# Kernel optimization log

Measured on AMD Instinct MI355X. Metric: run time of the kernel, lower is better.

## Reference

```python
import jax, jax.numpy as jnp
import numpy as np

BN_EPS = 1e-5

def _square_distance(src, dst):
    # src: (B,N,3), dst: (B,S,3) -> (B,N,S)
    d = -2.0 * jnp.einsum('bnc,bsc->bns', src, dst)
    d = d + jnp.sum(src * src, -1)[:, :, None]
    d = d + jnp.sum(dst * dst, -1)[:, None, :]
    return d

def _bn_relu(x, gamma, beta):
    # x: (B,N,C); training-mode batchnorm over (B,N)
    mean = jnp.mean(x, axis=(0, 1))
    var = jnp.mean(jnp.square(x - mean), axis=(0, 1))
    y = (x - mean) * jax.lax.rsqrt(var + BN_EPS) * gamma + beta
    return jax.nn.relu(y)

def setup_inputs() -> dict:
    key = jax.random.key(0)
    ks = jax.random.split(key, 12)
    B, N, S, D1, D2 = 8, 8192, 2048, 128, 256
    in_ch, mlp = 384, [256, 256]
    inp = {
        'xyz1': jax.random.normal(ks[0], (B, 3, N), jnp.float32),
        'xyz2': jax.random.normal(ks[1], (B, 3, S), jnp.float32),
        'points1': jax.random.normal(ks[2], (B, D1, N), jnp.float32),
        'points2': jax.random.normal(ks[3], (B, D2, S), jnp.float32),
    }
    last = in_ch
    for i, out in enumerate(mlp):
        inp[f'W{i+1}'] = jax.random.normal(ks[4 + 2 * i], (out, last), jnp.float32) * (1.0 / np.sqrt(last))
        inp[f'b{i+1}'] = jnp.zeros((out,), jnp.float32)
        inp[f'g{i+1}'] = jnp.ones((out,), jnp.float32)
        inp[f'beta{i+1}'] = jnp.zeros((out,), jnp.float32)
        last = out
    return inp

def reference(xyz1, xyz2, points1, points2, W1, b1, g1, beta1, W2, b2, g2, beta2):
    p1 = jnp.transpose(xyz1, (0, 2, 1))   # (B,N,3)
    p2 = jnp.transpose(xyz2, (0, 2, 1))   # (B,S,3)
    f2 = jnp.transpose(points2, (0, 2, 1))  # (B,S,D2)

    dists = _square_distance(p1, p2)      # (B,N,S)
    neg_d, idx = jax.lax.top_k(-dists, 3)  # 3 smallest distances
    d3 = -neg_d                            # (B,N,3)
    dist_recip = 1.0 / (d3 + 1e-8)
    weight = dist_recip / jnp.sum(dist_recip, axis=2, keepdims=True)  # (B,N,3)

    gathered = jax.vmap(lambda p, i: p[i])(f2, idx)   # (B,N,3,D2)
    interp = jnp.sum(gathered * weight[..., None], axis=2)  # (B,N,D2)

    f1 = jnp.transpose(points1, (0, 2, 1))  # (B,N,D1)
    x = jnp.concatenate([f1, interp], axis=-1)  # (B,N,D1+D2)

    x = _bn_relu(jnp.einsum('bnc,oc->bno', x, W1) + b1, g1, beta1)
    x = _bn_relu(jnp.einsum('bnc,oc->bno', x, W2) + b2, g2, beta2)
    return jnp.transpose(x, (0, 2, 1))  # (B,256,N)
```

## Files before the change

### kernel.cpp

```cpp
#include <hip/hip_runtime.h>

#define B_   8
#define N_   8192
#define S_   2048
#define D1_  128
#define D2_  256
#define O_   256
#define BN_  (B_*N_)

typedef __bf16 bf16;
typedef __bf16 bf16x8_t __attribute__((ext_vector_type(8)));
typedef __bf16 bf16x4_t __attribute__((ext_vector_type(4)));
typedef float  f32x4_t  __attribute__((ext_vector_type(4)));

static const size_t OFF_IDX  = 0;
static const size_t OFF_W    = 786432;
static const size_t OFF_XP   = 1572864;
static const size_t OFF_Z    = 51904512;
static const size_t OFF_SS1  = 85458944;
static const size_t OFF_SS2  = 85460992;
static const size_t OFF_PART = 85463040;

#define GL16(gsrc, ldst) \
  __builtin_amdgcn_global_load_lds((const __attribute__((address_space(1))) void*)(gsrc), \
                                   (__attribute__((address_space(3))) void*)(ldst), 16, 0, 0)

__global__ __launch_bounds__(256) void k_conv_p1(const float* __restrict__ p1, bf16* __restrict__ xp) {
  const int g  = blockIdx.x * 256 + threadIdx.x;
  const int n4 = g & 2047;
  const int c8 = (g >> 11) & 15;
  const int b  = g >> 15;
  const int n  = n4 * 4;
  const float* src = p1 + ((size_t)b * D1_ + c8 * 8) * N_ + n;
  bf16x8_t o0, o1, o2, o3;
  #pragma unroll
  for (int j = 0; j < 8; ++j) {
    float4 v = *(const float4*)(src + (size_t)j * N_);
    o0[j] = (bf16)v.x; o1[j] = (bf16)v.y; o2[j] = (bf16)v.z; o3[j] = (bf16)v.w;
  }
  bf16* dst = xp + (((size_t)b * 48 + c8) * N_ + n) * 8;
  *(bf16x8_t*)(dst)      = o0;
  *(bf16x8_t*)(dst + 8)  = o1;
  *(bf16x8_t*)(dst + 16) = o2;
  *(bf16x8_t*)(dst + 24) = o3;
}

__device__ __forceinline__ void ins3(float d, int i,
                                     float& d0, float& d1, float& d2,
                                     int& i0, int& i1, int& i2) {
  const bool c2 = d < d2, c1 = d < d1, c0 = d < d0;
  const float nd2 = c1 ? d1 : (c2 ? d : d2); const int ni2 = c1 ? i1 : (c2 ? i : i2);
  const float nd1 = c0 ? d0 : (c1 ? d : d1); const int ni1 = c0 ? i0 : (c1 ? i : i1);
  d0 = c0 ? d : d0; i0 = c0 ? i : i0;
  d1 = nd1; i1 = ni1; d2 = nd2; i2 = ni2;
}

__global__ __launch_bounds__(256) void k_nn3(const float* __restrict__ xyz1, const float* __restrict__ xyz2,
                                             int* __restrict__ idxw, float* __restrict__ www) {
  __shared__ float4 sq[4][S_ / 4];
  __shared__ float  pd[4][64][3];
  __shared__ int    pi[4][64][3];
  const int tid  = threadIdx.x;
  const int lane = tid & 63, w = tid >> 6;
  const int b     = blockIdx.y;
  const int nbase = blockIdx.x * 64;

  const float* x2 = xyz2 + (size_t)b * 3 * S_;
  for (int j = tid; j < S_ / 4; j += 256) {
    const float4 x = *(const float4*)(x2 + 4 * j);
    const float4 y = *(const float4*)(x2 + S_ + 4 * j);
    const float4 z = *(const float4*)(x2 + 2 * S_ + 4 * j);
    float4 qq;
    qq.x = fmaf(x.x, x.x, fmaf(y.x, y.x, z.x * z.x));
    qq.y = fmaf(x.y, x.y, fmaf(y.y, y.y, z.y * z.y));
    qq.z = fmaf(x.z, x.z, fmaf(y.z, y.z, z.z * z.z));
    qq.w = fmaf(x.w, x.w, fmaf(y.w, y.w, z.w * z.w));
    sq[0][j] = x; sq[1][j] = y; sq[2][j] = z; sq[3][j] = qq;
  }

  const int n = nbase + lane;
  const float* x1 = xyz1 + (size_t)b * 3 * N_;
  const float px = x1[n], py = x1[N_ + n], pz = x1[2 * N_ + n];
  const float ax = -2.f * px, ay = -2.f * py, az = -2.f * pz;
  __syncthreads();

  float e0 = 3.4e38f, e1 = 3.4e38f, e2 = 3.4e38f;
  int   i0 = 0, i1 = 0, i2 = 0;

  const int jb = w * (S_ / 16);
  #pragma unroll 4
  for (int j = jb; j < jb + S_ / 16; ++j) {
    const float4 qx = sq[0][j], qy = sq[1][j], qz = sq[2][j], qq = sq[3][j];
    #define CAND(C, SI)                                                        \
      {                                                                        \
        const float E = fmaf(ax, qx.C, fmaf(ay, qy.C, fmaf(az, qz.C, qq.C))); \
        const bool l0 = E < e0, l1 = E < e1, l2 = E < e2;                      \
        const int ni1 = l0 ? i0 : (l1 ? (SI) : i1);                            \
        const int ni2 = l1 ? i1 : (l2 ? (SI) : i2);                            \
        i0 = l0 ? (SI) : i0; i1 = ni1; i2 = ni2;                               \
        const float ne1 = __builtin_amdgcn_fmed3f(E, e0, e1);                  \
        const float ne2 = __builtin_amdgcn_fmed3f(E, e1, e2);                  \
        e0 = fminf(E, e0); e1 = ne1; e2 = ne2;                                 \
      }
    CAND(x, 4 * j + 0)
    CAND(y, 4 * j + 1)
    CAND(z, 4 * j + 2)
    CAND(w, 4 * j + 3)
    #undef CAND
  }

  const float pp = fmaf(px, px, fmaf(py, py, pz * pz));
  pd[w][lane][0] = e0 + pp; pd[w][lane][1] = e1 + pp; pd[w][lane][2] = e2 + pp;
  pi[w][lane][0] = i0; pi[w][lane][1] = i1; pi[w][lane][2] = i2;
  __syncthreads();

  if (tid < 64) {
    float d0 = pd[0][tid][0], d1 = pd[0][tid][1], d2 = pd[0][tid][2];
    int   j0 = pi[0][tid][0], j1 = pi[0][tid][1], j2 = pi[0][tid][2];
    #pragma unroll
    for (int ck = 1; ck < 4; ++ck)
      #pragma unroll
      for (int k = 0; k < 3; ++k)
        ins3(pd[ck][tid][k], pi[ck][tid][k], d0, d1, d2, j0, j1, j2);
    const float r0 = 1.f / (d0 + 1e-8f), r1 = 1.f / (d1 + 1e-8f), r2 = 1.f / (d2 + 1e-8f);
    const float inv = 1.f / (r0 + r1 + r2);
    const int bn = b * N_ + nbase + tid;
    idxw[bn] = j0; idxw[BN_ + bn] = j1; idxw[2 * BN_ + bn] = j2;
    www[bn] = r0 * inv; www[BN_ + bn] = r1 * inv; www[2 * BN_ + bn] = r2 * inv;
  }
}

__global__ __launch_bounds__(256) void k_t2(const float* __restrict__ p2, bf16* __restrict__ f2t) {
  __shared__ float lds[64][65];
  const int bid = blockIdx.x;
  const int b = bid & 7;
  const int inner = bid >> 3;
  const int s0 = (inner & 31) * 64;
  const int c0 = (inner >> 5) * 64;
  const int t = threadIdx.x;
  {
    const int cr = t >> 2, scb = (t & 3) * 16;
    const float* src = p2 + ((size_t)b * D2_ + c0 + cr) * S_ + s0 + scb;
    #pragma unroll
    for (int i = 0; i < 4; ++i) {
      const float4 v = *(const float4*)(src + 4 * i);
      lds[cr][scb + 4 * i + 0] = v.x; lds[cr][scb + 4 * i + 1] = v.y;
      lds[cr][scb + 4 * i + 2] = v.z; lds[cr][scb + 4 * i + 3] = v.w;
    }
  }
  __syncthreads();
  const int co = (t & 7) * 8;
  #pragma unroll
  for (int pass = 0; pass < 2; ++pass) {
    const int s = pass * 32 + (t >> 3);
    bf16x8_t o;
    #pragma unroll
    for (int j = 0; j < 8; ++j) o[j] = (bf16)lds[co + j][s];
    *(bf16x8_t*)(f2t + ((size_t)b * S_ + s0 + s) * D2_ + c0 + co) = o;
  }
}

__global__ __launch_bounds__(256) void k_interp(const bf16* __restrict__ f2t, const int* __restrict__ idxw,
                                                const float* __restrict__ www, bf16* __restrict__ xp) {
  const int bid = blockIdx.x;
  const int b = bid & 7;
  const int n = (bid >> 3) * 8 + (threadIdx.x & 7);
  const int c8 = threadIdx.x >> 3;
  const int bn = b * N_ + n;
  const int j0 = idxw[bn], j1 = idxw[BN_ + bn], j2 = idxw[2 * BN_ + bn];
  const float w0 = www[bn], w1 = www[BN_ + bn], w2 = www[2 * BN_ + bn];
  const bf16* base = f2t + (size_t)b * S_ * D2_ + c8 * 8;
  const bf16x8_t v0 = *(const bf16x8_t*)(base + (size_t)j0 * D2_);
  const bf16x8_t v1 = *(const bf16x8_t*)(base + (size_t)j1 * D2_);
  const bf16x8_t v2 = *(const bf16x8_t*)(base + (size_t)j2 * D2_);
  bf16x8_t out;
  #pragma unroll
  for (int j = 0; j < 8; ++j)
    out[j] = (bf16)(w0 * (float)v0[j] + w1 * (float)v1[j] + w2 * (float)v2[j]);
  *(bf16x8_t*)(xp + (((size_t)b * 48 + 16 + c8) * N_ + (size_t)n) * 8) = out;
}

__global__ __launch_bounds__(256) void k_wprep(const float* __restrict__ W1, const float* __restrict__ W2,
                                               bf16* __restrict__ img) {
  const int g = blockIdx.x * 256 + threadIdx.x;
  if (g < 12288) {
    const int e = g * 8;
    const int imgblk = e >> 12, r = e & 4095;
    const int kc = r >> 10, row = (r & 1023) >> 3;
    const int mblk = imgblk / 12, kt32 = imgblk % 12;
    const float* s = W1 + (size_t)(mblk * 128 + row) * 384 + kt32 * 32 + kc * 8;
    const float4 f0 = *(const float4*)(s), f1 = *(const float4*)(s + 4);
    bf16x8_t h;
    h[0] = (bf16)f0.x; h[1] = (bf16)f0.y; h[2] = (bf16)f0.z; h[3] = (bf16)f0.w;
    h[4] = (bf16)f1.x; h[5] = (bf16)f1.y; h[6] = (bf16)f1.z; h[7] = (bf16)f1.w;
    *(bf16x8_t*)(img + e) = h;
  } else if (g < 20480) {
    const int e = (g - 12288) * 8;
    const int imgblk = e >> 12, r = e & 4095;
    const int kc = r >> 10, row = (r & 1023) >> 3;
    const int mblk = imgblk >> 3, kt32 = imgblk & 7;
    const float* s = W2 + (size_t)(mblk * 128 + row) * 256 + kt32 * 32 + kc * 8;
    const float4 f0 = *(const float4*)(s), f1 = *(const float4*)(s + 4);
    bf16x8_t h;
    h[0] = (bf16)f0.x; h[1] = (bf16)f0.y; h[2] = (bf16)f0.z; h[3] = (bf16)f0.w;
    h[4] = (bf16)f1.x; h[5] = (bf16)f1.y; h[6] = (bf16)f1.z; h[7] = (bf16)f1.w;
    *(bf16x8_t*)(img + 98304 + e) = h;
  }
}

template<int K>
__global__ __launch_bounds__(256) void k_gemm(const bf16* __restrict__ Wimg, const float* __restrict__ bias,
                                              const bf16* __restrict__ X, bf16* __restrict__ Zp) {
  __shared__ bf16 As[4096];
  __shared__ bf16 Bt[4096];
  const int tid = threadIdx.x;
  const int lane = tid & 63, wid = tid >> 6;
  const int wr = wid >> 1, wc = wid & 1;
  const int dd = blockIdx.x;
  const int xcd = dd & 7, pos = dd >> 3;
  const int b = pos >> 4, q = pos & 15;
  const int m0 = (q & 1) * 128;
  const int n0 = (xcd * 8 + (q >> 1)) * 128;
  const int mblk = m0 >> 7;
  const int l15 = lane & 15, l4 = lane >> 4;

  f32x4_t acc[4][4];
  #pragma unroll
  for (int i = 0; i < 4; ++i)
    #pragma unroll
    for (int j = 0; j < 4; ++j) { f32x4_t z = {0.f, 0.f, 0.f, 0.f}; acc[i][j] = z; }

  const bf16* Xb = X + (size_t)b * (K / 8) * ((size_t)N_ * 8);

  for (int kt = 0; kt < K; kt += 32) {
    const bf16* asrc = Wimg + (size_t)(mblk * (K / 32) + (kt >> 5)) * 4096 + wid * 1024 + lane * 8;
    GL16(asrc,       &As[wid * 1024]);
    GL16(asrc + 512, &As[wid * 1024 + 512]);
    const bf16* bsrc = Xb + ((size_t)(kt >> 3) + wid) * ((size_t)N_ * 8) + ((size_t)n0 + lane) * 8;
    GL16(bsrc,       &Bt[wid * 1024]);
    GL16(bsrc + 512, &Bt[wid * 1024 + 512]);
    __syncthreads();
    bf16x8_t af[4], bfr[4];
    #pragma unroll
    for (int mi = 0; mi < 4; ++mi) af[mi]  = *(const bf16x8_t*)&As[l4 * 1024 + (wr * 64 + mi * 16 + l15) * 8];
    #pragma unroll
    for (int ni = 0; ni < 4; ++ni) bfr[ni] = *(const bf16x8_t*)&Bt[l4 * 1024 + (wc * 64 + ni * 16 + l15) * 8];
    #pragma unroll
    for (int mi = 0; mi < 4; ++mi)
      #pragma unroll
      for (int ni = 0; ni < 4; ++ni)
        acc[mi][ni] = __builtin_amdgcn_mfma_f32_16x16x32_bf16(af[mi], bfr[ni], acc[mi][ni], 0, 0, 0);
    __syncthreads();
  }
  bf16* Zb = Zp + (size_t)b * 32 * ((size_t)N_ * 8);
  #pragma unroll
  for (int mi = 0; mi < 4; ++mi) {
    const int obase = m0 + wr * 64 + mi * 16 + l4 * 4;
    const float4 bv = *(const float4*)(bias + obase);
    const size_t gofs = (size_t)(obase >> 3) * ((size_t)N_ * 8) + (obase & 7);
    #pragma unroll
    for (int ni = 0; ni < 4; ++ni) {
      const int nn = n0 + wc * 64 + ni * 16 + l15;
      bf16x4_t o;
      o[0] = (bf16)(acc[mi][ni][0] + bv.x);
      o[1] = (bf16)(acc[mi][ni][1] + bv.y);
      o[2] = (bf16)(acc[mi][ni][2] + bv.z);
      o[3] = (bf16)(acc[mi][ni][3] + bv.w);
      *(bf16x4_t*)(Zb + gofs + (size_t)nn * 8) = o;
    }
  }
}

__global__ __launch_bounds__(256) void k_stats_p(const bf16* __restrict__ Z, float* __restrict__ part) {
  const int og = blockIdx.x & 31, b = blockIdx.x >> 5;
  const bf16* src = Z + ((size_t)b * 32 + og) * ((size_t)N_ * 8);
  float s[8], q[8];
  #pragma unroll
  for (int j = 0; j < 8; ++j) { s[j] = 0.f; q[j] = 0.f; }
  for (int n = threadIdx.x; n < N_; n += 256) {
    const bf16x8_t v = *(const bf16x8_t*)(src + (size_t)n * 8);
    #pragma unroll
    for (int j = 0; j < 8; ++j) {
      const float f = (float)v[j];
      s[j] += f; q[j] = fmaf(f, f, q[j]);
    }
  }
  #pragma unroll
  for (int off = 1; off < 64; off <<= 1) {
    #pragma unroll
    for (int j = 0; j < 8; ++j) {
      s[j] += __shfl_xor(s[j], off);
      q[j] += __shfl_xor(q[j], off);
    }
  }
  __shared__ float red[4][16];
  const int w = threadIdx.x >> 6;
  if ((threadIdx.x & 63) == 0) {
    #pragma unroll
    for (int j = 0; j < 8; ++j) { red[w][j] = s[j]; red[w][8 + j] = q[j]; }
  }
  __syncthreads();
  if (threadIdx.x < 16) {
    const float t = red[0][threadIdx.x] + red[1][threadIdx.x] + red[2][threadIdx.x] + red[3][threadIdx.x];
    const int sel = threadIdx.x >> 3, j = threadIdx.x & 7;
    part[((size_t)sel * 256 + og * 8 + j) * 8 + b] = t;
  }
}

__global__ __launch_bounds__(256) void k_ss(const float* __restrict__ part, const float* __restrict__ g,
                                            const float* __restrict__ be, float* __restrict__ ss) {
  const int c = threadIdx.x;
  float s = 0.f, q = 0.f;
  #pragma unroll
  for (int b = 0; b < 8; ++b) { s += part[(size_t)c * 8 + b]; q += part[(256 + (size_t)c) * 8 + b]; }
  const float mean = s * (1.f / 65536.f);
  const float var  = q * (1.f / 65536.f) - mean * mean;
  const float rstd = rsqrtf(var + 1e-5f);
  const float sc = g[c] * rstd;
  ss[c] = sc; ss[O_ + c] = be[c] - mean * sc;
}

__global__ __launch_bounds__(256) void k_apply_p(bf16* __restrict__ Z, const float* __restrict__ ss) {
  const int nc = blockIdx.x & 31, og = (blockIdx.x >> 5) & 31, b = blockIdx.x >> 10;
  const int n = nc * 256 + threadIdx.x;
  bf16* p = Z + (((size_t)b * 32 + og) * N_ + n) * 8;
  bf16x8_t v = *(bf16x8_t*)p;
  #pragma unroll
  for (int j = 0; j < 8; ++j) {
    const int c = og * 8 + j;
    v[j] = (bf16)fmaxf(fmaf((float)v[j], ss[c], ss[O_ + c]), 0.f);
  }
  *(bf16x8_t*)p = v;
}

__global__ __launch_bounds__(256) void k_final_p(const bf16* __restrict__ Z, const float* __restrict__ ss,
                                                 float* __restrict__ Y) {
  const int b  = blockIdx.x >> 7;
  const int n0 = (blockIdx.x & 127) * 64;
  const int og = threadIdx.x >> 3, ns = threadIdx.x & 7;
  const bf16* src = Z + (((size_t)b * 32 + og) * N_ + n0 + ns * 8) * 8;
  bf16x8_t v[8];
  #pragma unroll
  for (int i = 0; i < 8; ++i) v[i] = *(const bf16x8_t*)(src + i * 8);
  float sc[8], sh[8];
  #pragma unroll
  for (int j = 0; j < 8; ++j) { sc[j] = ss[og * 8 + j]; sh[j] = ss[O_ + og * 8 + j]; }
  float* dst = Y + ((size_t)b * O_ + og * 8) * N_ + n0 + ns * 8;
  #pragma unroll
  for (int j = 0; j < 8; ++j) {
    float4 a0, a1;
    a0.x = fmaxf(fmaf((float)v[0][j], sc[j], sh[j]), 0.f);
    a0.y = fmaxf(fmaf((float)v[1][j], sc[j], sh[j]), 0.f);
    a0.z = fmaxf(fmaf((float)v[2][j], sc[j], sh[j]), 0.f);
    a0.w = fmaxf(fmaf((float)v[3][j], sc[j], sh[j]), 0.f);
    a1.x = fmaxf(fmaf((float)v[4][j], sc[j], sh[j]), 0.f);
    a1.y = fmaxf(fmaf((float)v[5][j], sc[j], sh[j]), 0.f);
    a1.z = fmaxf(fmaf((float)v[6][j], sc[j], sh[j]), 0.f);
    a1.w = fmaxf(fmaf((float)v[7][j], sc[j], sh[j]), 0.f);
    *(float4*)(dst + (size_t)j * N_)     = a0;
    *(float4*)(dst + (size_t)j * N_ + 4) = a1;
  }
}

extern "C" void kernel_launch(void* const* d_in, const int* in_sizes, int n_in,
                              void* d_out, int out_size, void* d_ws, size_t ws_size,
                              hipStream_t stream) {
  const float* xyz1    = (const float*)d_in[0];
  const float* xyz2    = (const float*)d_in[1];
  const float* points1 = (const float*)d_in[2];
  const float* points2 = (const float*)d_in[3];
  const float* W1  = (const float*)d_in[4];
  const float* b1  = (const float*)d_in[5];
  const float* g1  = (const float*)d_in[6];
  const float* be1 = (const float*)d_in[7];
  const float* W2  = (const float*)d_in[8];
  const float* b2  = (const float*)d_in[9];
  const float* g2  = (const float*)d_in[10];
  const float* be2 = (const float*)d_in[11];
  float* Y = (float*)d_out;
  char*  ws = (char*)d_ws;
  int*   idxw  = (int*)(ws + OFF_IDX);
  float* www   = (float*)(ws + OFF_W);
  bf16*  wimg1 = (bf16*)(ws + OFF_IDX);
  bf16*  wimg2 = wimg1 + 98304;
  bf16*  xp    = (bf16*)(ws + OFF_XP);
  bf16*  z1    = (bf16*)(ws + OFF_Z);
  bf16*  f2t   = (bf16*)(ws + OFF_Z);
  bf16*  z2    = (bf16*)(ws + OFF_XP);
  float* ss1   = (float*)(ws + OFF_SS1);
  float* ss2   = (float*)(ws + OFF_SS2);
  float* part  = (float*)(ws + OFF_PART);

  hipLaunchKernelGGL(k_conv_p1, dim3(1024), dim3(256), 0, stream, points1, xp);
  hipLaunchKernelGGL(k_nn3, dim3(128, 8), dim3(256), 0, stream, xyz1, xyz2, idxw, www);
  hipLaunchKernelGGL(k_t2, dim3(1024), dim3(256), 0, stream, points2, f2t);
  hipLaunchKernelGGL(k_interp, dim3(8192), dim3(256), 0, stream, f2t, idxw, www, xp);
  hipLaunchKernelGGL(k_wprep, dim3(80), dim3(256), 0, stream, W1, W2, wimg1);
  hipLaunchKernelGGL((k_gemm<384>), dim3(1024), dim3(256), 0, stream, wimg1, b1, xp, z1);
  hipLaunchKernelGGL(k_stats_p, dim3(256), dim3(256), 0, stream, z1, part);
  hipLaunchKernelGGL(k_ss, dim3(1), dim3(256), 0, stream, part, g1, be1, ss1);
  hipLaunchKernelGGL(k_apply_p, dim3(8192), dim3(256), 0, stream, z1, ss1);
  hipLaunchKernelGGL((k_gemm<256>), dim3(1024), dim3(256), 0, stream, wimg2, b2, z1, z2);
  hipLaunchKernelGGL(k_stats_p, dim3(256), dim3(256), 0, stream, z2, part);
  hipLaunchKernelGGL(k_ss, dim3(1), dim3(256), 0, stream, part, g2, be2, ss2);
  hipLaunchKernelGGL(k_final_p, dim3(1024), dim3(256), 0, stream, z2, ss2, Y);
}
```

Before: 190.8 us.

## Replace brute-force 3-NN with z-binned spatial search and pruning

Adds a per-batch kernel that buckets xyz2 points into 64 z-slabs (counting sort), then rewrites the 3-NN kernel to search outward from the query's slab and stop once the slab distance exceeds the current third-best distance. The goal is to avoid evaluating all 2048 candidates per query point. It packs distance and index into 64-bit keys for the top-3 selection. In exchange it adds an extra launch and divergent, data-dependent loops, and the pruning gain depends on the point distribution. Ties are broken by index, and distances are now computed directly rather than through the expanded-norm formula, so they may differ slightly from the reference.

```diff
diff --git a/kernel.cpp b/kernel.cpp
--- a/kernel.cpp
+++ b/kernel.cpp
@@ -45,87 +45,139 @@
   *(bf16x8_t*)(dst + 24) = o3;
 }
 
-__device__ __forceinline__ void ins3(float d, int i,
-                                     float& d0, float& d1, float& d2,
-                                     int& i0, int& i1, int& i2) {
-  const bool c2 = d < d2, c1 = d < d1, c0 = d < d0;
-  const float nd2 = c1 ? d1 : (c2 ? d : d2); const int ni2 = c1 ? i1 : (c2 ? i : i2);
-  const float nd1 = c0 ? d0 : (c1 ? d : d1); const int ni1 = c0 ? i0 : (c1 ? i : i1);
-  d0 = c0 ? d : d0; i0 = c0 ? i : i0;
-  d1 = nd1; i1 = ni1; d2 = nd2; i2 = ni2;
-}
-
-__global__ __launch_bounds__(256) void k_nn3(const float* __restrict__ xyz1, const float* __restrict__ xyz2,
+__global__ __launch_bounds__(256) void k_sortz(const float* __restrict__ xyz2,
+                                               float4* __restrict__ srt, int* __restrict__ hdr) {
+  __shared__ float zl[S_];
+  __shared__ int cnt[64], cnt2[64], starts[65];
+  __shared__ float rmin[4], rmax[4];
+  const int b = blockIdx.x, tid = threadIdx.x;
+  const float* z2 = xyz2 + (size_t)b * 3 * S_ + 2 * S_;
+  float lmin = 3.4e38f, lmax = -3.4e38f;
+  for (int i = tid; i < S_; i += 256) {
+    const float z = z2[i]; zl[i] = z;
+    lmin = fminf(lmin, z); lmax = fmaxf(lmax, z);
+  }
+  #pragma unroll
+  for (int off = 32; off; off >>= 1) {
+    lmin = fminf(lmin, __shfl_down(lmin, off));
+    lmax = fmaxf(lmax, __shfl_down(lmax, off));
+  }
+  if ((tid & 63) == 0) { rmin[tid >> 6] = lmin; rmax[tid >> 6] = lmax; }
+  if (tid < 64) { cnt[tid] = 0; cnt2[tid] = 0; }
+  __syncthreads();
+  const float zmin = fminf(fminf(rmin[0], rmin[1]), fminf(rmin[2], rmin[3]));
+  const float zmax = fmaxf(fmaxf(rmax[0], rmax[1]), fmaxf(rmax[2], rmax[3]));
+  const float scale = 63.999f / fmaxf(zmax - zmin, 1e-20f);
+  for (int i = tid; i < S_; i += 256) {
+    const int bi = min(63, max(0, (int)((zl[i] - zmin) * scale)));
+    atomicAdd(&cnt[bi], 1);
+  }
+  __syncthreads();
+  if (tid == 0) {
+    int acc = 0;
+    for (int k = 0; k < 64; ++k) { starts[k] = acc; acc += cnt[k]; }
+    starts[64] = acc;
+  }
+  __syncthreads();
+  const float* x2 = xyz2 + (size_t)b * 3 * S_;
+  const float* y2 = x2 + S_;
+  for (int i = tid; i < S_; i += 256) {
+    const float z = zl[i];
+    const int bi = min(63, max(0, (int)((z - zmin) * scale)));
+    const int pos = starts[bi] + atomicAdd(&cnt2[bi], 1);
+    float4 o; o.x = x2[i]; o.y = y2[i]; o.z = z; o.w = __uint_as_float((unsigned)i);
+    srt[(size_t)b * S_ + pos] = o;
+  }
+  if (tid < 65) hdr[b * 68 + tid] = starts[tid];
+  if (tid == 0) { hdr[b * 68 + 65] = __float_as_int(zmin); hdr[b * 68 + 66] = __float_as_int(scale); }
+}
+
+__global__ __launch_bounds__(256) void k_nn3(const float* __restrict__ xyz1, const float4* __restrict__ srt_g,
+                                             const int* __restrict__ hdr,
                                              int* __restrict__ idxw, float* __restrict__ www) {
-  __shared__ float4 sq[4][S_ / 4];
-  __shared__ float  pd[4][64][3];
-  __shared__ int    pi[4][64][3];
-  const int tid  = threadIdx.x;
-  const int lane = tid & 63, w = tid >> 6;
-  const int b     = blockIdx.y;
-  const int nbase = blockIdx.x * 64;
-
-  const float* x2 = xyz2 + (size_t)b * 3 * S_;
-  for (int j = tid; j < S_ / 4; j += 256) {
-    const float4 x = *(const float4*)(x2 + 4 * j);
-    const float4 y = *(const float4*)(x2 + S_ + 4 * j);
-    const float4 z = *(const float4*)(x2 + 2 * S_ + 4 * j);
-    float4 qq;
-    qq.x = fmaf(x.x, x.x, fmaf(y.x, y.x, z.x * z.x));
-    qq.y = fmaf(x.y, x.y, fmaf(y.y, y.y, z.y * z.y));
-    qq.z = fmaf(x.z, x.z, fmaf(y.z, y.z, z.z * z.z));
-    qq.w = fmaf(x.w, x.w, fmaf(y.w, y.w, z.w * z.w));
-    sq[0][j] = x; sq[1][j] = y; sq[2][j] = z; sq[3][j] = qq;
-  }
+  __shared__ float4 srt[S_];
+  __shared__ int starts_l[65];
+  __shared__ unsigned long long pk[4][64][3];
+  const int tid = threadIdx.x, lane = tid & 63, w = tid >> 6;
+  const int b = blockIdx.y, nbase = blockIdx.x * 64;
+
+  const float4* sg = srt_g + (size_t)b * S_;
+  for (int i = tid; i < S_; i += 256) srt[i] = sg[i];
+  if (tid < 65) starts_l[tid] = hdr[b * 68 + tid];
+  const float zmin  = __int_as_float(hdr[b * 68 + 65]);
+  const float scale = __int_as_float(hdr[b * 68 + 66]);
 
   const int n = nbase + lane;
   const float* x1 = xyz1 + (size_t)b * 3 * N_;
   const float px = x1[n], py = x1[N_ + n], pz = x1[2 * N_ + n];
-  const float ax = -2.f * px, ay = -2.f * py, az = -2.f * pz;
-  __syncthreads();
-
-  float e0 = 3.4e38f, e1 = 3.4e38f, e2 = 3.4e38f;
-  int   i0 = 0, i1 = 0, i2 = 0;
-
-  const int jb = w * (S_ / 16);
-  #pragma unroll 4
-  for (int j = jb; j < jb + S_ / 16; ++j) {
-    const float4 qx = sq[0][j], qy = sq[1][j], qz = sq[2][j], qq = sq[3][j];
-    #define CAND(C, SI)                                                        \
-      {                                                                        \
-        const float E = fmaf(ax, qx.C, fmaf(ay, qy.C, fmaf(az, qz.C, qq.C))); \
-        const bool l0 = E < e0, l1 = E < e1, l2 = E < e2;                      \
-        const int ni1 = l0 ? i0 : (l1 ? (SI) : i1);                            \
-        const int ni2 = l1 ? i1 : (l2 ? (SI) : i2);                            \
-        i0 = l0 ? (SI) : i0; i1 = ni1; i2 = ni2;                               \
-        const float ne1 = __builtin_amdgcn_fmed3f(E, e0, e1);                  \
-        const float ne2 = __builtin_amdgcn_fmed3f(E, e1, e2);                  \
-        e0 = fminf(E, e0); e1 = ne1; e2 = ne2;                                 \
-      }
-    CAND(x, 4 * j + 0)
-    CAND(y, 4 * j + 1)
-    CAND(z, 4 * j + 2)
-    CAND(w, 4 * j + 3)
-    #undef CAND
-  }
-
-  const float pp = fmaf(px, px, fmaf(py, py, pz * pz));
-  pd[w][lane][0] = e0 + pp; pd[w][lane][1] = e1 + pp; pd[w][lane][2] = e2 + pp;
-  pi[w][lane][0] = i0; pi[w][lane][1] = i1; pi[w][lane][2] = i2;
+  __syncthreads();
+
+  const float winv   = 1.f / scale;
+  const float winv_p = winv * 1.000002f;
+  const float winv_m = winv * 0.999998f;
+  const int qb = min(63, max(0, (int)((pz - zmin) * scale)));
+
+  unsigned long long k0 = 0x7F7FFFFFFFFFFFFFull, k1 = k0, k2 = k0;
+
+  int lo = qb, hi = qb, cur = qb;
+  bool have = true;
+  for (int round = 0; round < 66; ++round) {
+    const int curc = min(63, max(0, cur));
+    const int s = starts_l[curc];
+    const int cnt = have ? (starts_l[curc + 1] - s) : 0;
+    for (int t = 0; ; ++t) {
+      const int e = w + 4 * t;
+      const bool v = e < cnt;
+      if (!__any(v)) break;
+      const float4 c = srt[s + (v ? e : 0)];
+      const float dx = px - c.x, dy = py - c.y, dzv = pz - c.z;
+      const float d = fmaf(dx, dx, fmaf(dy, dy, dzv * dzv));
+      unsigned long long key = ((unsigned long long)__float_as_uint(d) << 32)
+                             | (unsigned long long)__float_as_uint(c.w);
+      if (!v) key = ~0ull;
+      const bool c0 = key < k0, c1 = key < k1, c2 = key < k2;
+      const unsigned long long n1 = c0 ? k0 : (c1 ? key : k1);
+      const unsigned long long n2 = c1 ? k1 : (c2 ? key : k2);
+      k0 = c0 ? key : k0; k1 = n1; k2 = n2;
+    }
+    const float d2  = __uint_as_float((unsigned)(k2 >> 32));
+    const float dzl = (lo > 0)  ? (pz - fmaf((float)lo, winv_p, zmin)) : 3.4e38f;
+    const float dzr = (hi < 63) ? (fmaf((float)(hi + 1), winv_m, zmin) - pz) : 3.4e38f;
+    const bool goL = (lo > 0)  && (dzl * dzl <= d2);
+    const bool goR = (hi < 63) && (dzr * dzr <= d2);
+    const bool pickL = goL && (!goR || dzl <= dzr);
+    const bool pickR = goR && !pickL;
+    have = pickL || pickR;
+    cur = pickL ? (lo - 1) : (hi + 1);
+    lo -= pickL ? 1 : 0;
+    hi += pickR ? 1 : 0;
+    if (!__any(have)) break;
+  }
+
+  pk[w][lane][0] = k0; pk[w][lane][1] = k1; pk[w][lane][2] = k2;
   __syncthreads();
 
   if (tid < 64) {
-    float d0 = pd[0][tid][0], d1 = pd[0][tid][1], d2 = pd[0][tid][2];
-    int   j0 = pi[0][tid][0], j1 = pi[0][tid][1], j2 = pi[0][tid][2];
+    unsigned long long m0 = pk[0][tid][0], m1 = pk[0][tid][1], m2 = pk[0][tid][2];
     #pragma unroll
     for (int ck = 1; ck < 4; ++ck)
       #pragma unroll
-      for (int k = 0; k < 3; ++k)
-        ins3(pd[ck][tid][k], pi[ck][tid][k], d0, d1, d2, j0, j1, j2);
+      for (int k = 0; k < 3; ++k) {
+        const unsigned long long key = pk[ck][tid][k];
+        const bool c0 = key < m0, c1 = key < m1, c2 = key < m2;
+        const unsigned long long n1 = c0 ? m0 : (c1 ? key : m1);
+        const unsigned long long n2 = c1 ? m1 : (c2 ? key : m2);
+        m0 = c0 ? key : m0; m1 = n1; m2 = n2;
+      }
+    const float d0 = __uint_as_float((unsigned)(m0 >> 32));
+    const float d1 = __uint_as_float((unsigned)(m1 >> 32));
+    const float d2 = __uint_as_float((unsigned)(m2 >> 32));
     const float r0 = 1.f / (d0 + 1e-8f), r1 = 1.f / (d1 + 1e-8f), r2 = 1.f / (d2 + 1e-8f);
     const float inv = 1.f / (r0 + r1 + r2);
     const int bn = b * N_ + nbase + tid;
-    idxw[bn] = j0; idxw[BN_ + bn] = j1; idxw[2 * BN_ + bn] = j2;
+    idxw[bn]           = (int)(unsigned)(m0 & 0xFFFFFFFFull);
+    idxw[BN_ + bn]     = (int)(unsigned)(m1 & 0xFFFFFFFFull);
+    idxw[2 * BN_ + bn] = (int)(unsigned)(m2 & 0xFFFFFFFFull);
     www[bn] = r0 * inv; www[BN_ + bn] = r1 * inv; www[2 * BN_ + bn] = r2 * inv;
   }
 }
@@ -384,6 +436,8 @@
   bf16*  wimg1 = (bf16*)(ws + OFF_IDX);
   bf16*  wimg2 = wimg1 + 98304;
   bf16*  xp    = (bf16*)(ws + OFF_XP);
+  float4* srt  = (float4*)(ws + OFF_Z);
+  int*    hdr  = (int*)(ws + OFF_Z + 262144);
   bf16*  z1    = (bf16*)(ws + OFF_Z);
   bf16*  f2t   = (bf16*)(ws + OFF_Z);
   bf16*  z2    = (bf16*)(ws + OFF_XP);
@@ -392,7 +446,8 @@
   float* part  = (float*)(ws + OFF_PART);
 
   hipLaunchKernelGGL(k_conv_p1, dim3(1024), dim3(256), 0, stream, points1, xp);
-  hipLaunchKernelGGL(k_nn3, dim3(128, 8), dim3(256), 0, stream, xyz1, xyz2, idxw, www);
+  hipLaunchKernelGGL(k_sortz, dim3(8), dim3(256), 0, stream, xyz2, srt, hdr);
+  hipLaunchKernelGGL(k_nn3, dim3(128, 8), dim3(256), 0, stream, xyz1, srt, hdr, idxw, www);
   hipLaunchKernelGGL(k_t2, dim3(1024), dim3(256), 0, stream, points2, f2t);
   hipLaunchKernelGGL(k_interp, dim3(8192), dim3(256), 0, stream, f2t, idxw, www, xp);
   hipLaunchKernelGGL(k_wprep, dim3(80), dim3(256), 0, stream, W1, W2, wimg1);
```

After: 286.5 us. +50.2%, slower.

## Replace brute-force 3-NN with z-slab binned search over sorted points

Applied to the files above, without the earlier changes.

Adds two kernels that counting-sort reference and query points into 64 z-slabs per batch, then rewrites the 3-NN kernel so each wavefront scans only a window of slabs near its sorted queries. The window expands until the third-best distance proves no closer point can exist outside it. This removes most of the all-pairs distance work, at the cost of two extra small-grid sort kernels with serial per-thread loops and some wavefront divergence in the window expansion.

```diff
diff --git a/kernel.cpp b/kernel.cpp
--- a/kernel.cpp
+++ b/kernel.cpp
@@ -17,6 +17,9 @@
 static const size_t OFF_W    = 786432;
 static const size_t OFF_XP   = 1572864;
 static const size_t OFF_Z    = 51904512;
+static const size_t OFF_CS   = OFF_Z;
+static const size_t OFF_HDR  = OFF_Z + 327680;
+static const size_t OFF_QS   = OFF_Z + 331776;
 static const size_t OFF_SS1  = 85458944;
 static const size_t OFF_SS2  = 85460992;
 static const size_t OFF_PART = 85463040;
@@ -45,89 +48,209 @@
   *(bf16x8_t*)(dst + 24) = o3;
 }
 
-__device__ __forceinline__ void ins3(float d, int i,
-                                     float& d0, float& d1, float& d2,
-                                     int& i0, int& i1, int& i2) {
-  const bool c2 = d < d2, c1 = d < d1, c0 = d < d0;
-  const float nd2 = c1 ? d1 : (c2 ? d : d2); const int ni2 = c1 ? i1 : (c2 ? i : i2);
-  const float nd1 = c0 ? d0 : (c1 ? d : d1); const int ni1 = c0 ? i0 : (c1 ? i : i1);
-  d0 = c0 ? d : d0; i0 = c0 ? i : i0;
-  d1 = nd1; i1 = ni1; d2 = nd2; i2 = ni2;
-}
-
-__global__ __launch_bounds__(256) void k_nn3(const float* __restrict__ xyz1, const float* __restrict__ xyz2,
+__global__ __launch_bounds__(256) void k_sortz(const float* __restrict__ xyz2,
+                                               float* __restrict__ cs, int* __restrict__ hdr) {
+  __shared__ float zl[S_];
+  __shared__ unsigned short h[64][257];
+  __shared__ int starts[65];
+  __shared__ float mm[8];
+  const int b = blockIdx.x, t = threadIdx.x;
+  const float* x2 = xyz2 + (size_t)b * 3 * S_;
+  const float* y2 = x2 + S_;
+  const float* z2 = x2 + 2 * S_;
+  float lmin = 3.4e38f, lmax = -3.4e38f;
+  for (int i = t; i < S_; i += 256) {
+    const float z = z2[i]; zl[i] = z;
+    lmin = fminf(lmin, z); lmax = fmaxf(lmax, z);
+  }
+  #pragma unroll
+  for (int off = 32; off; off >>= 1) {
+    lmin = fminf(lmin, __shfl_down(lmin, off));
+    lmax = fmaxf(lmax, __shfl_down(lmax, off));
+  }
+  if ((t & 63) == 0) { mm[t >> 6] = lmin; mm[4 + (t >> 6)] = lmax; }
+  unsigned short* hf = &h[0][0];
+  for (int i = t; i < 64 * 257; i += 256) hf[i] = 0;
+  __syncthreads();
+  const float zmin  = fminf(fminf(mm[0], mm[1]), fminf(mm[2], mm[3]));
+  const float zmax  = fmaxf(fmaxf(mm[4], mm[5]), fmaxf(mm[6], mm[7]));
+  const float scale = 63.999f / fmaxf(zmax - zmin, 1e-20f);
+  #pragma unroll
+  for (int k = 0; k < 8; ++k) {
+    const int i = t * 8 + k;
+    const int bi = min(63, (int)((zl[i] - zmin) * scale));
+    h[bi][t]++;
+  }
+  __syncthreads();
+  if (t < 64) {
+    int run = 0;
+    for (int tt = 0; tt < 256; ++tt) { const int c = h[t][tt]; h[t][tt] = (unsigned short)run; run += c; }
+    starts[t] = run;
+  }
+  __syncthreads();
+  if (t == 0) {
+    int acc = 0;
+    for (int k = 0; k < 64; ++k) { const int c = starts[k]; starts[k] = acc; acc += c; }
+    starts[64] = acc;
+  }
+  __syncthreads();
+  float* xs = cs + (size_t)b * 5 * S_;
+  float* ys = xs + S_; float* zs = ys + S_; float* qs = zs + S_; float* ids = qs + S_;
+  #pragma unroll
+  for (int k = 0; k < 8; ++k) {
+    const int i = t * 8 + k;
+    const float z = zl[i];
+    const int bi = min(63, (int)((z - zmin) * scale));
+    const int pos = starts[bi] + h[bi][t]; h[bi][t]++;
+    const float x = x2[i], y = y2[i];
+    xs[pos] = x; ys[pos] = y; zs[pos] = z;
+    qs[pos] = fmaf(x, x, fmaf(y, y, z * z));
+    ids[pos] = __uint_as_float((unsigned)i);
+  }
+  if (t < 65) hdr[b * 68 + t] = starts[t];
+  if (t == 0) { hdr[b * 68 + 65] = __float_as_int(zmin); hdr[b * 68 + 66] = __float_as_int(scale); }
+}
+
+__global__ __launch_bounds__(256) void k_sortq(const float* __restrict__ xyz1, float4* __restrict__ qsrt) {
+  __shared__ unsigned short h[64][257];
+  __shared__ int starts[65];
+  __shared__ float mm[8];
+  const int b = blockIdx.x, t = threadIdx.x;
+  const float* x1 = xyz1 + (size_t)b * 3 * N_;
+  const float* y1 = x1 + N_;
+  const float* z1 = x1 + 2 * N_;
+  float lmin = 3.4e38f, lmax = -3.4e38f;
+  for (int i = t; i < N_; i += 256) {
+    const float z = z1[i];
+    lmin = fminf(lmin, z); lmax = fmaxf(lmax, z);
+  }
+  #pragma unroll
+  for (int off = 32; off; off >>= 1) {
+    lmin = fminf(lmin, __shfl_down(lmin, off));
+    lmax = fmaxf(lmax, __shfl_down(lmax, off));
+  }
+  if ((t & 63) == 0) { mm[t >> 6] = lmin; mm[4 + (t >> 6)] = lmax; }
+  unsigned short* hf = &h[0][0];
+  for (int i = t; i < 64 * 257; i += 256) hf[i] = 0;
+  __syncthreads();
+  const float zmin  = fminf(fminf(mm[0], mm[1]), fminf(mm[2], mm[3]));
+  const float zmax  = fmaxf(fmaxf(mm[4], mm[5]), fmaxf(mm[6], mm[7]));
+  const float scale = 63.999f / fmaxf(zmax - zmin, 1e-20f);
+  for (int k = 0; k < 32; ++k) {
+    const int i = t * 32 + k;
+    const int bi = min(63, (int)((z1[i] - zmin) * scale));
+    h[bi][t]++;
+  }
+  __syncthreads();
+  if (t < 64) {
+    int run = 0;
+    for (int tt = 0; tt < 256; ++tt) { const int c = h[t][tt]; h[t][tt] = (unsigned short)run; run += c; }
+    starts[t] = run;
+  }
+  __syncthreads();
+  if (t == 0) {
+    int acc = 0;
+    for (int k = 0; k < 64; ++k) { const int c = starts[k]; starts[k] = acc; acc += c; }
+    starts[64] = acc;
+  }
+  __syncthreads();
+  for (int k = 0; k < 32; ++k) {
+    const int i = t * 32 + k;
+    const float z = z1[i];
+    const int bi = min(63, (int)((z - zmin) * scale));
+    const int pos = starts[bi] + h[bi][t]; h[bi][t]++;
+    float4 o; o.x = x1[i]; o.y = y1[i]; o.z = z; o.w = __uint_as_float((unsigned)i);
+    qsrt[(size_t)b * N_ + pos] = o;
+  }
+}
+
+#define CAND(C, SI)                                                            \
+  {                                                                            \
+    const float E = fmaf(ax, qx.C, fmaf(ay, qy.C, fmaf(az, qz.C, qv.C)));      \
+    const bool l0 = E < e0, l1 = E < e1, l2 = E < e2;                          \
+    const int t1 = l0 ? s0 : (l1 ? (SI) : s1);                                 \
+    const int t2 = l1 ? s1 : (l2 ? (SI) : s2);                                 \
+    s0 = l0 ? (SI) : s0; s1 = t1; s2 = t2;                                     \
+    const float m1 = __builtin_amdgcn_fmed3f(E, e0, e1);                       \
+    const float m2 = __builtin_amdgcn_fmed3f(E, e1, e2);                       \
+    e0 = fminf(E, e0); e1 = m1; e2 = m2;                                       \
+  }
+#define SCAN_RANGE(GA, GB)                                                     \
+  for (int j_ = (GA); j_ < (GB); ++j_) {                                       \
+    const float4 qx = sq[0][j_], qy = sq[1][j_], qz = sq[2][j_], qv = sq[3][j_]; \
+    CAND(x, 4 * j_)                                                            \
+    CAND(y, 4 * j_ + 1)                                                        \
+    CAND(z, 4 * j_ + 2)                                                        \
+    CAND(w, 4 * j_ + 3)                                                        \
+  }
+
+__global__ __launch_bounds__(256) void k_nn3(const float4* __restrict__ qsrt, const float* __restrict__ cs,
+                                             const int* __restrict__ hdr,
                                              int* __restrict__ idxw, float* __restrict__ www) {
-  __shared__ float4 sq[4][S_ / 4];
-  __shared__ float  pd[4][64][3];
-  __shared__ int    pi[4][64][3];
-  const int tid  = threadIdx.x;
-  const int lane = tid & 63, w = tid >> 6;
-  const int b     = blockIdx.y;
-  const int nbase = blockIdx.x * 64;
-
-  const float* x2 = xyz2 + (size_t)b * 3 * S_;
-  for (int j = tid; j < S_ / 4; j += 256) {
-    const float4 x = *(const float4*)(x2 + 4 * j);
-    const float4 y = *(const float4*)(x2 + S_ + 4 * j);
-    const float4 z = *(const float4*)(x2 + 2 * S_ + 4 * j);
-    float4 qq;
-    qq.x = fmaf(x.x, x.x, fmaf(y.x, y.x, z.x * z.x));
-    qq.y = fmaf(x.y, x.y, fmaf(y.y, y.y, z.y * z.y));
-    qq.z = fmaf(x.z, x.z, fmaf(y.z, y.z, z.z * z.z));
-    qq.w = fmaf(x.w, x.w, fmaf(y.w, y.w, z.w * z.w));
-    sq[0][j] = x; sq[1][j] = y; sq[2][j] = z; sq[3][j] = qq;
-  }
-
-  const int n = nbase + lane;
-  const float* x1 = xyz1 + (size_t)b * 3 * N_;
-  const float px = x1[n], py = x1[N_ + n], pz = x1[2 * N_ + n];
+  __shared__ float4 sq[5][512];
+  __shared__ int starts_l[65];
+  const int tid = threadIdx.x;
+  const int b = blockIdx.y, qbase = blockIdx.x * 256;
+
+  const float4* cs4 = (const float4*)(cs + (size_t)b * 5 * S_);
+  for (int g = tid; g < 5 * 512; g += 256) sq[g >> 9][g & 511] = cs4[g];
+  if (tid < 65) starts_l[tid] = hdr[b * 68 + tid];
+  const float zmin  = __int_as_float(hdr[b * 68 + 65]);
+  const float scale = __int_as_float(hdr[b * 68 + 66]);
+
+  const float4 q = qsrt[(size_t)b * N_ + qbase + tid];
+  const float px = q.x, py = q.y, pz = q.z;
+  const unsigned qn = __float_as_uint(q.w);
   const float ax = -2.f * px, ay = -2.f * py, az = -2.f * pz;
-  __syncthreads();
+  const float pp = fmaf(px, px, fmaf(py, py, pz * pz));
+  __syncthreads();
+
+  const float winv = 1.f / scale;
+  const int qb = min(63, max(0, (int)((pz - zmin) * scale)));
+  int loB = qb, hiB = qb;
+  while (loB > 0  && (starts_l[qb] - starts_l[loB])     < 256) --loB;
+  while (hiB < 63 && (starts_l[hiB + 1] - starts_l[qb + 1]) < 256) ++hiB;
+  #pragma unroll
+  for (int off = 1; off < 64; off <<= 1) {
+    loB = min(loB, __shfl_xor(loB, off));
+    hiB = max(hiB, __shfl_xor(hiB, off));
+  }
+  int gl = starts_l[loB] >> 2;
+  int gh = (starts_l[hiB + 1] + 3) >> 2;
 
   float e0 = 3.4e38f, e1 = 3.4e38f, e2 = 3.4e38f;
-  int   i0 = 0, i1 = 0, i2 = 0;
-
-  const int jb = w * (S_ / 16);
-  #pragma unroll 4
-  for (int j = jb; j < jb + S_ / 16; ++j) {
-    const float4 qx = sq[0][j], qy = sq[1][j], qz = sq[2][j], qq = sq[3][j];
-    #define CAND(C, SI)                                                        \
-      {                                                                        \
-        const float E = fmaf(ax, qx.C, fmaf(ay, qy.C, fmaf(az, qz.C, qq.C))); \
-        const bool l0 = E < e0, l1 = E < e1, l2 = E < e2;                      \
-        const int ni1 = l0 ? i0 : (l1 ? (SI) : i1);                            \
-        const int ni2 = l1 ? i1 : (l2 ? (SI) : i2);                            \
-        i0 = l0 ? (SI) : i0; i1 = ni1; i2 = ni2;                               \
-        const float ne1 = __builtin_amdgcn_fmed3f(E, e0, e1);                  \
-        const float ne2 = __builtin_amdgcn_fmed3f(E, e1, e2);                  \
-        e0 = fminf(E, e0); e1 = ne1; e2 = ne2;                                 \
-      }
-    CAND(x, 4 * j + 0)
-    CAND(y, 4 * j + 1)
-    CAND(z, 4 * j + 2)
-    CAND(w, 4 * j + 3)
-    #undef CAND
-  }
-
-  const float pp = fmaf(px, px, fmaf(py, py, pz * pz));
-  pd[w][lane][0] = e0 + pp; pd[w][lane][1] = e1 + pp; pd[w][lane][2] = e2 + pp;
-  pi[w][lane][0] = i0; pi[w][lane][1] = i1; pi[w][lane][2] = i2;
-  __syncthreads();
-
-  if (tid < 64) {
-    float d0 = pd[0][tid][0], d1 = pd[0][tid][1], d2 = pd[0][tid][2];
-    int   j0 = pi[0][tid][0], j1 = pi[0][tid][1], j2 = pi[0][tid][2];
-    #pragma unroll
-    for (int ck = 1; ck < 4; ++ck)
-      #pragma unroll
-      for (int k = 0; k < 3; ++k)
-        ins3(pd[ck][tid][k], pi[ck][tid][k], d0, d1, d2, j0, j1, j2);
-    const float r0 = 1.f / (d0 + 1e-8f), r1 = 1.f / (d1 + 1e-8f), r2 = 1.f / (d2 + 1e-8f);
-    const float inv = 1.f / (r0 + r1 + r2);
-    const int bn = b * N_ + nbase + tid;
-    idxw[bn] = j0; idxw[BN_ + bn] = j1; idxw[2 * BN_ + bn] = j2;
-    www[bn] = r0 * inv; www[BN_ + bn] = r1 * inv; www[2 * BN_ + bn] = r2 * inv;
-  }
+  int s0 = 0, s1 = 0, s2 = 0;
+  SCAN_RANGE(gl, gh)
+
+  for (int it = 0; it < 80; ++it) {
+    float d2c = e2 + pp; d2c = d2c + fabsf(d2c) * 2e-6f + 1e-10f;
+    bool nl = false, nr = false;
+    if (loB > 0) {
+      const float edge = fmaf((float)loB, winv * 1.000002f, zmin);
+      const float dz = pz - edge;
+      nl = !(dz > 0.f && dz * dz * 0.999998f > d2c);
+    }
+    if (hiB < 63) {
+      const float edge = fmaf((float)(hiB + 1), winv * 0.999998f, zmin);
+      const float dz = edge - pz;
+      nr = !(dz > 0.f && dz * dz * 0.999998f > d2c);
+    }
+    const bool el = __any(nl), er = __any(nr);
+    if (!el && !er) break;
+    if (el) { const int nb = max(0, loB - 2);  const int ng = starts_l[nb] >> 2;        SCAN_RANGE(ng, gl) gl = ng; loB = nb; }
+    if (er) { const int nb = min(63, hiB + 2); const int ng = (starts_l[nb + 1] + 3) >> 2; SCAN_RANGE(gh, ng) gh = ng; hiB = nb; }
+  }
+
+  const float* idsf = (const float*)&sq[4][0];
+  const int i0 = (int)__float_as_uint(idsf[s0]);
+  const int i1 = (int)__float_as_uint(idsf[s1]);
+  const int i2 = (int)__float_as_uint(idsf[s2]);
+  const float d0 = e0 + pp, d1 = e1 + pp, d2v = e2 + pp;
+  const float r0 = 1.f / (d0 + 1e-8f), r1 = 1.f / (d1 + 1e-8f), r2 = 1.f / (d2v + 1e-8f);
+  const float inv = 1.f / (r0 + r1 + r2);
+  const int bn = b * N_ + (int)qn;
+  idxw[bn] = i0; idxw[BN_ + bn] = i1; idxw[2 * BN_ + bn] = i2;
+  www[bn] = r0 * inv; www[BN_ + bn] = r1 * inv; www[2 * BN_ + bn] = r2 * inv;
 }
 
 __global__ __launch_bounds__(256) void k_t2(const float* __restrict__ p2, bf16* __restrict__ f2t) {
@@ -384,6 +507,9 @@
   bf16*  wimg1 = (bf16*)(ws + OFF_IDX);
   bf16*  wimg2 = wimg1 + 98304;
   bf16*  xp    = (bf16*)(ws + OFF_XP);
+  float* cs    = (float*)(ws + OFF_CS);
+  int*   hdr   = (int*)(ws + OFF_HDR);
+  float4* qsrt = (float4*)(ws + OFF_QS);
   bf16*  z1    = (bf16*)(ws + OFF_Z);
   bf16*  f2t   = (bf16*)(ws + OFF_Z);
   bf16*  z2    = (bf16*)(ws + OFF_XP);
@@ -392,7 +518,9 @@
   float* part  = (float*)(ws + OFF_PART);
 
   hipLaunchKernelGGL(k_conv_p1, dim3(1024), dim3(256), 0, stream, points1, xp);
-  hipLaunchKernelGGL(k_nn3, dim3(128, 8), dim3(256), 0, stream, xyz1, xyz2, idxw, www);
+  hipLaunchKernelGGL(k_sortz, dim3(8), dim3(256), 0, stream, xyz2, cs, hdr);
+  hipLaunchKernelGGL(k_sortq, dim3(8), dim3(256), 0, stream, xyz1, qsrt);
+  hipLaunchKernelGGL(k_nn3, dim3(32, 8), dim3(256), 0, stream, qsrt, cs, hdr, idxw, www);
   hipLaunchKernelGGL(k_t2, dim3(1024), dim3(256), 0, stream, points2, f2t);
   hipLaunchKernelGGL(k_interp, dim3(8192), dim3(256), 0, stream, f2t, idxw, www, xp);
   hipLaunchKernelGGL(k_wprep, dim3(80), dim3(256), 0, stream, W1, W2, wimg1);
```

After: 253.7 us. 1.33x slower.
